# Kernel optimization log

Measured on AMD Instinct MI355X. Metric: run time of the kernel, lower is better.

## Reference

```python
import jax, jax.numpy as jnp
import numpy as np

B, T, D, R = 8, 4096, 512, 1024  # batch, tokens, dim, merges per sequence


def setup_inputs() -> dict:
    key = jax.random.key(0)
    k1, k2 = jax.random.split(key, 2)
    x = jax.random.normal(k1, (B, T, D), jnp.float32)
    W = jax.random.normal(k2, (D, D), jnp.float32) * (1.0 / np.sqrt(D))
    b = jnp.zeros((D,), jnp.float32)
    return {"x": x, "W": W, "b": b}


def _l2norm(v):
    # matches torch F.normalize(p=2, eps=1e-12)
    return v / jnp.maximum(jnp.linalg.norm(v, axis=-1, keepdims=True), 1e-12)


def _scatter_rows(arr, idx, vals):
    # arr: (B, T, d); idx: (B, r); vals: (B, r, d) -> set rows along axis 1
    Bn, _, d = arr.shape
    return arr.at[jnp.arange(Bn)[:, None, None], idx[:, :, None], jnp.arange(d)[None, None, :]].set(vals)


def _tome_forward(x, W, b, r):
    Bn, Tn, d = x.shape
    dst = x[:, 0::2, :]   # even positions
    src = x[:, 1::2, :]   # odd positions
    # cosine similarity bipartite scores: (B, T/2, T/2)
    scores = jnp.einsum('bsd,btd->bst', _l2norm(src), _l2norm(dst))
    best_scores = scores.max(axis=-1)          # (B, T_src)
    best_local = scores.argmax(axis=-1)        # (B, T_src)
    _, top_src = jax.lax.top_k(best_scores, r) # (B, r) src tokens with strongest match
    src_idx = top_src * 2 + 1                  # odd original positions
    dst_idx = jnp.take_along_axis(best_local, top_src, axis=1) * 2  # even original positions
    bidx = jnp.arange(Bn)[:, None]
    merged_away = jnp.zeros((Bn, Tn), bool).at[bidx, src_idx].set(True)

    # --- merge: average src into matched dst, drop src rows ---
    src_vals = jnp.take_along_axis(x, src_idx[:, :, None], axis=1)
    dst_vals = jnp.take_along_axis(x, dst_idx[:, :, None], axis=1)
    x_out = _scatter_rows(x, dst_idx, (src_vals + dst_vals) * 0.5)
    # kept positions in ascending order (stable sort: False before True)
    col = jnp.argsort(merged_away, axis=1, stable=True)[:, :Tn - r]  # (B, T-r)
    merged = jnp.take_along_axis(x_out, col[:, :, None], axis=1)     # (B, T-r, d)

    # --- wrapped dense layer ---
    hidden = merged @ W + b

    # --- unmerge: scatter kept rows back, copy dst value into src slots ---
    out = _scatter_rows(jnp.zeros((Bn, Tn, d), x.dtype), col, hidden)
    dvals = jnp.take_along_axis(out, dst_idx[:, :, None], axis=1)
    out = _scatter_rows(out, src_idx, dvals)
    return out


def reference(x, W, b):
    return _tome_forward(x, W, b, R)
```

## Files before the change

### kernel.cpp

```cpp
#include <hip/hip_runtime.h>
#include <stdint.h>

#define NB   8
#define TOK  4096
#define DIM  512
#define HALF 2048
#define RR   1024

typedef unsigned long long u64;
typedef unsigned int u32;
typedef _Float16 f16;
typedef f16 f16x4 __attribute__((ext_vector_type(4)));
typedef f16 f16x8 __attribute__((ext_vector_type(8)));
typedef float f32x4 __attribute__((ext_vector_type(4)));

#define AS1 __attribute__((address_space(1)))
#define AS3 __attribute__((address_space(3)))
#define GLL16(GP, LP) __builtin_amdgcn_global_load_lds((const AS1 u32*)(GP), (AS3 u32*)(LP), 16, 0, 0)

__device__ __forceinline__ u32 mono_f32(float f) {
    u32 u = __float_as_uint(f);
    return (u & 0x80000000u) ? ~u : (u | 0x80000000u);
}
__device__ __forceinline__ u64 umax64(u64 a, u64 b) { return a > b ? a : b; }

__global__ void k_init(u64* __restrict__ best, u64* __restrict__ wkey) {
    int i = blockIdx.x * 256 + threadIdx.x;
    if (i < NB * HALF) { best[i] = 0ull; wkey[i] = ~0ull; }
}

__global__ void k_prep(const float* __restrict__ x, f16* __restrict__ xh, f16* __restrict__ xl,
                       float* __restrict__ invn) {
    int row  = blockIdx.x * 4 + (threadIdx.x >> 6);
    int lane = threadIdx.x & 63;
    const float* p = x + (size_t)row * DIM + 4 * lane;
    float4 v0 = *(const float4*)p;
    float4 v1 = *(const float4*)(p + 256);
    float va[8] = {v0.x, v0.y, v0.z, v0.w, v1.x, v1.y, v1.z, v1.w};
    f16x4 h0, h1, l0, l1;
#pragma unroll
    for (int e = 0; e < 4; ++e) {
        f16 hh = (f16)va[e];     h0[e] = hh; l0[e] = (f16)(va[e] - (float)hh);
        f16 hh1 = (f16)va[e+4];  h1[e] = hh1; l1[e] = (f16)(va[e+4] - (float)hh1);
    }
    size_t off = (size_t)row * DIM + 4 * lane;
    *(f16x4*)(xh + off)       = h0;
    *(f16x4*)(xh + off + 256) = h1;
    *(f16x4*)(xl + off)       = l0;
    *(f16x4*)(xl + off + 256) = l1;
    float ss = va[0]*va[0] + va[1]*va[1] + va[2]*va[2] + va[3]*va[3]
             + va[4]*va[4] + va[5]*va[5] + va[6]*va[6] + va[7]*va[7];
#pragma unroll
    for (int m = 32; m; m >>= 1) ss += __shfl_xor(ss, m, 64);
    if (lane == 0) invn[row] = 1.0f / fmaxf(sqrtf(ss), 1e-12f);
}

__global__ void k_wsplit(const float* __restrict__ W, f16* __restrict__ Wh, f16* __restrict__ Wl) {
    __shared__ float tile[64][65];
    int k0 = (blockIdx.x >> 3) * 64, n0 = (blockIdx.x & 7) * 64;
    int t = threadIdx.x;
#pragma unroll
    for (int i = 0; i < 16; ++i) {
        int idx = t + 256 * i;
        int r = idx >> 6, c = idx & 63;
        tile[r][c] = W[(size_t)(k0 + r) * DIM + n0 + c];
    }
    __syncthreads();
#pragma unroll
    for (int i = 0; i < 16; ++i) {
        int idx = t + 256 * i;
        int n = idx >> 6, k = idx & 63;
        float v = tile[k][n];
        f16 h = (f16)v;
        Wh[(size_t)(n0 + n) * DIM + k0 + k] = h;
        Wl[(size_t)(n0 + n) * DIM + k0 + k] = (f16)(v - (float)h);
    }
}

__launch_bounds__(256)
__global__ void k_scores(const f16* __restrict__ xh, const f16* __restrict__ xl,
                         const float* __restrict__ invn, u64* __restrict__ best) {
    __shared__ f16 As[128][64];
    __shared__ f16 Bs[128][64];
    int bx = blockIdx.x;
    int b = bx >> 8, sb = (bx >> 4) & 15, tb = bx & 15;
    int tid = threadIdx.x, lane = tid & 63, w = tid >> 6, wr = w >> 1, wc = w & 1;
    int cc = lane >> 4, rm = lane & 15, rm7 = rm & 7;
    f16* Asl = &As[0][0];
    f16* Bsl = &Bs[0][0];

    f32x4 acc[4][4];
#pragma unroll
    for (int i = 0; i < 4; ++i)
#pragma unroll
        for (int j = 0; j < 4; ++j) acc[i][j] = (f32x4){0.f, 0.f, 0.f, 0.f};

    size_t rowA[4], rowB[4];
#pragma unroll
    for (int r = 0; r < 4; ++r) {
        int g = tid + 256 * r;
        int m = g >> 3;
        int chunk = (g & 7) ^ (m & 7);
        rowA[r] = ((size_t)b * TOK + 2 * (sb * 128 + m) + 1) * DIM + 8 * chunk;
        rowB[r] = ((size_t)b * TOK + 2 * (tb * 128 + m)    ) * DIM + 8 * chunk;
    }

    for (int ks = 0; ks < 24; ++ks) {
        int third = ks >> 3, col0 = (ks & 7) << 6;
        const f16* Aa = (third == 1) ? xl : xh;
        const f16* Ba = (third == 2) ? xl : xh;
#pragma unroll
        for (int r = 0; r < 4; ++r) {
            GLL16(Aa + rowA[r] + col0, Asl + (size_t)(256 * r + 64 * w) * 8);
            GLL16(Ba + rowB[r] + col0, Bsl + (size_t)(256 * r + 64 * w) * 8);
        }
        __syncthreads();
        const f16* Abase = Asl + (wr * 64 + rm) * 64;
        const f16* Bbase = Bsl + (wc * 64 + rm) * 64;
#pragma unroll
        for (int kk = 0; kk < 2; ++kk) {
            f16x8 af[4], bf[4];
            int ex = 8 * ((kk * 4 + cc) ^ rm7);
#pragma unroll
            for (int f = 0; f < 4; ++f) {
                af[f] = *(const f16x8*)(Abase + f * 1024 + ex);
                bf[f] = *(const f16x8*)(Bbase + f * 1024 + ex);
            }
#pragma unroll
            for (int i = 0; i < 4; ++i)
#pragma unroll
                for (int j = 0; j < 4; ++j)
                    acc[i][j] = __builtin_amdgcn_mfma_f32_16x16x32_f16(af[i], bf[j], acc[i][j], 0, 0, 0);
        }
        __syncthreads();
    }

    float invd[4];
#pragma unroll
    for (int j = 0; j < 4; ++j) {
        int t = tb * 128 + wc * 64 + j * 16 + rm;
        invd[j] = invn[(size_t)b * TOK + 2 * t];
    }
#pragma unroll
    for (int i = 0; i < 4; ++i) {
#pragma unroll
        for (int r = 0; r < 4; ++r) {
            int s = sb * 128 + wr * 64 + i * 16 + cc * 4 + r;
            float invs = invn[(size_t)b * TOK + 2 * s + 1];
            u64 key = 0;
#pragma unroll
            for (int j = 0; j < 4; ++j) {
                int t = tb * 128 + wc * 64 + j * 16 + rm;
                float sc = acc[i][j][r] * invs * invd[j];
                u64 k = ((u64)mono_f32(sc) << 32) | (u32)(2047 - t);
                key = umax64(key, k);
            }
#pragma unroll
            for (int m = 1; m < 16; m <<= 1) {
                u32 lo = (u32)key, hi = (u32)(key >> 32);
                lo = __shfl_xor(lo, m, 64);
                hi = __shfl_xor(hi, m, 64);
                key = umax64(key, ((u64)hi << 32) | lo);
            }
            if (rm == 0) atomicMax(&best[b * HALF + s], key);
        }
    }
}

__global__ void k_topk(const u64* __restrict__ best, u64* __restrict__ wkey,
                       u32* __restrict__ member, u32* __restrict__ dstmap) {
    __shared__ u32 smono[HALF];
    int b = blockIdx.x >> 4, sc = blockIdx.x & 15;
    int tid = threadIdx.x;
#pragma unroll
    for (int r = 0; r < 8; ++r) { int s = r * 256 + tid; smono[s] = (u32)(best[b * HALF + s] >> 32); }
    __syncthreads();
    int s = sc * 128 + (tid >> 1);
    u32 ms = smono[s];
    int t0 = (tid & 1) * 1024;
    int cnt = 0;
    for (int t = t0; t < t0 + 1024; ++t) {
        u32 mt = smono[t];
        cnt += ((mt > ms) || (mt == ms && t < s)) ? 1 : 0;
    }
    int oth = __shfl_xor(cnt, 1, 64);
    if ((tid & 1) == 0) {
        int rank = cnt + oth;
        u64 k = best[b * HALF + s];
        u32 d = 2047u - (u32)(k & 0xffffffffu);
        dstmap[b * HALF + s] = d;
        u32 mem = (rank < RR) ? 1u : 0u;
        member[b * HALF + s] = mem;
        if (mem) {
            u64 key = (k & 0xffffffff00000000ull) | (u32)(2047 - s);
            atomicMin(&wkey[b * HALF + d], key);
        }
    }
}

__global__ void k_merge2(const float* __restrict__ x, const u64* __restrict__ wkey,
                         f16* __restrict__ xh, f16* __restrict__ xl) {
    int idx = blockIdx.x;
    int b = idx >> 11, d = idx & (HALF - 1);
    u64 wk = wkey[b * HALF + d];
    if (wk == ~0ull) return;
    int s = 2047 - (int)(wk & 0xffffffffu);
    const float* xd = x + ((size_t)b * TOK + 2 * d) * DIM;
    const float* xs = x + ((size_t)b * TOK + 2 * s + 1) * DIM;
    int l0 = threadIdx.x * 8;
    f16x8 h, l;
#pragma unroll
    for (int e = 0; e < 8; ++e) {
        float v = (xd[l0 + e] + xs[l0 + e]) * 0.5f;
        f16 hh = (f16)v;
        h[e] = hh;
        l[e] = (f16)(v - (float)hh);
    }
    size_t off = ((size_t)b * TOK + 2 * d) * DIM + l0;
    *(f16x8*)(xh + off) = h;
    *(f16x8*)(xl + off) = l;
}

__launch_bounds__(256)
__global__ void k_out(const f16* __restrict__ xh, const f16* __restrict__ xl,
                      const f16* __restrict__ Wh, const f16* __restrict__ Wl,
                      const float* __restrict__ bias, float* __restrict__ out) {
    __shared__ f16 As[128][64];
    __shared__ f16 Bs[128][64];
    int bx = blockIdx.x;
    int im = bx >> 2, in = bx & 3;
    int tid = threadIdx.x, lane = tid & 63, w = tid >> 6, wr = w >> 1, wc = w & 1;
    int cc = lane >> 4, rm = lane & 15, rm7 = rm & 7;
    f16* Asl = &As[0][0];
    f16* Bsl = &Bs[0][0];

    f32x4 acc[4][4];
#pragma unroll
    for (int i = 0; i < 4; ++i)
#pragma unroll
        for (int j = 0; j < 4; ++j) acc[i][j] = (f32x4){0.f, 0.f, 0.f, 0.f};

    size_t rowA[4], rowB[4];
#pragma unroll
    for (int r = 0; r < 4; ++r) {
        int g = tid + 256 * r;
        int m = g >> 3;
        int chunk = (g & 7) ^ (m & 7);
        rowA[r] = (size_t)(im * 128 + m) * DIM + 8 * chunk;
        rowB[r] = (size_t)(in * 128 + m) * DIM + 8 * chunk;
    }

    for (int ks = 0; ks < 24; ++ks) {
        int third = ks >> 3, col0 = (ks & 7) << 6;
        const f16* Aa = (third == 1) ? xl : xh;
        const f16* Ba = (third == 2) ? Wl : Wh;
#pragma unroll
        for (int r = 0; r < 4; ++r) {
            GLL16(Aa + rowA[r] + col0, Asl + (size_t)(256 * r + 64 * w) * 8);
            GLL16(Ba + rowB[r] + col0, Bsl + (size_t)(256 * r + 64 * w) * 8);
        }
        __syncthreads();
        const f16* Abase = Asl + (wr * 64 + rm) * 64;
        const f16* Bbase = Bsl + (wc * 64 + rm) * 64;
#pragma unroll
        for (int kk = 0; kk < 2; ++kk) {
            f16x8 af[4], bf[4];
            int ex = 8 * ((kk * 4 + cc) ^ rm7);
#pragma unroll
            for (int f = 0; f < 4; ++f) {
                af[f] = *(const f16x8*)(Abase + f * 1024 + ex);
                bf[f] = *(const f16x8*)(Bbase + f * 1024 + ex);
            }
#pragma unroll
            for (int i = 0; i < 4; ++i)
#pragma unroll
                for (int j = 0; j < 4; ++j)
                    acc[i][j] = __builtin_amdgcn_mfma_f32_16x16x32_f16(af[i], bf[j], acc[i][j], 0, 0, 0);
        }
        __syncthreads();
    }

    float bj[4];
#pragma unroll
    for (int j = 0; j < 4; ++j) bj[j] = bias[in * 128 + wc * 64 + j * 16 + rm];
#pragma unroll
    for (int i = 0; i < 4; ++i) {
#pragma unroll
        for (int r = 0; r < 4; ++r) {
            int gm = im * 128 + wr * 64 + i * 16 + cc * 4 + r;
#pragma unroll
            for (int j = 0; j < 4; ++j) {
                int n = in * 128 + wc * 64 + j * 16 + rm;
                out[(size_t)gm * DIM + n] = acc[i][j][r] + bj[j];
            }
        }
    }
}

__global__ void k_fix(const u32* __restrict__ member, const u32* __restrict__ dstmap,
                      float* __restrict__ out) {
    int idx = blockIdx.x;
    if (!member[idx]) return;
    int b = idx >> 11, s = idx & (HALF - 1);
    const float* sp = out + ((size_t)b * TOK + 2 * (size_t)dstmap[idx]) * DIM;
    float*       dp = out + ((size_t)b * TOK + 2 * (size_t)s + 1) * DIM;
    int l = threadIdx.x;
    *(float4*)(dp + 4 * l) = *(const float4*)(sp + 4 * l);
}

extern "C" void kernel_launch(void* const* d_in, const int* in_sizes, int n_in,
                              void* d_out, int out_size, void* d_ws, size_t ws_size,
                              hipStream_t stream) {
    const float* x    = (const float*)d_in[0];
    const float* W    = (const float*)d_in[1];
    const float* bias = (const float*)d_in[2];
    float* out = (float*)d_out;

    char* ws = (char*)d_ws;
    f16*   xh     = (f16*)(ws);
    f16*   xl     = (f16*)(ws + (32u << 20));
    f16*   Wh     = (f16*)(ws + (64u << 20));
    f16*   Wl     = (f16*)(ws + (64u << 20) + (512u << 10));
    float* invn   = (float*)(ws + (65u << 20));
    u64*   best   = (u64*)(ws + (65u << 20) + (128u << 10));
    u64*   wkey   = (u64*)(ws + (65u << 20) + (256u << 10));
    u32*   dstmap = (u32*)(ws + (65u << 20) + (384u << 10));
    u32*   member = (u32*)(ws + (65u << 20) + (448u << 10));

    hipLaunchKernelGGL(k_init,   dim3(64),    dim3(256), 0, stream, best, wkey);
    hipLaunchKernelGGL(k_prep,   dim3(8192),  dim3(256), 0, stream, x, xh, xl, invn);
    hipLaunchKernelGGL(k_wsplit, dim3(64),    dim3(256), 0, stream, W, Wh, Wl);
    hipLaunchKernelGGL(k_scores, dim3(2048),  dim3(256), 0, stream, xh, xl, invn, best);
    hipLaunchKernelGGL(k_topk,   dim3(128),   dim3(256), 0, stream, best, wkey, member, dstmap);
    hipLaunchKernelGGL(k_merge2, dim3(16384), dim3(64),  0, stream, x, wkey, xh, xl);
    hipLaunchKernelGGL(k_out,    dim3(1024),  dim3(256), 0, stream, xh, xl, Wh, Wl, bias, out);
    hipLaunchKernelGGL(k_fix,    dim3(16384), dim3(128), 0, stream, member, dstmap, out);
}
```

Baseline: 390.4 us.

## Double-buffer GEMM K-loops, fuse prep kernels, and fold unmerge copy into output GEMM

Merges the init, x-split and W-split kernels into one launch. Both GEMMs now stage the hi and lo halves of each K-slice together into double-buffered LDS, so the next slice loads while the current one computes, and one sync per step replaces the separate three-pass loop. The output GEMM also redirects each merged-away source row to read its dst row directly, which removes the k_fix pass. The cost is four times the LDS per block, which may reduce occupancy, and some duplicated GEMM rows for the redirected sources.

```diff
diff --git a/kernel.cpp b/kernel.cpp
--- a/kernel.cpp
+++ b/kernel.cpp
@@ -24,70 +24,100 @@
 }
 __device__ __forceinline__ u64 umax64(u64 a, u64 b) { return a > b ? a : b; }
 
-__global__ void k_init(u64* __restrict__ best, u64* __restrict__ wkey) {
-    int i = blockIdx.x * 256 + threadIdx.x;
-    if (i < NB * HALF) { best[i] = 0ull; wkey[i] = ~0ull; }
-}
-
-__global__ void k_prep(const float* __restrict__ x, f16* __restrict__ xh, f16* __restrict__ xl,
-                       float* __restrict__ invn) {
-    int row  = blockIdx.x * 4 + (threadIdx.x >> 6);
-    int lane = threadIdx.x & 63;
-    const float* p = x + (size_t)row * DIM + 4 * lane;
-    float4 v0 = *(const float4*)p;
-    float4 v1 = *(const float4*)(p + 256);
-    float va[8] = {v0.x, v0.y, v0.z, v0.w, v1.x, v1.y, v1.z, v1.w};
-    f16x4 h0, h1, l0, l1;
-#pragma unroll
-    for (int e = 0; e < 4; ++e) {
-        f16 hh = (f16)va[e];     h0[e] = hh; l0[e] = (f16)(va[e] - (float)hh);
-        f16 hh1 = (f16)va[e+4];  h1[e] = hh1; l1[e] = (f16)(va[e+4] - (float)hh1);
-    }
-    size_t off = (size_t)row * DIM + 4 * lane;
-    *(f16x4*)(xh + off)       = h0;
-    *(f16x4*)(xh + off + 256) = h1;
-    *(f16x4*)(xl + off)       = l0;
-    *(f16x4*)(xl + off + 256) = l1;
-    float ss = va[0]*va[0] + va[1]*va[1] + va[2]*va[2] + va[3]*va[3]
-             + va[4]*va[4] + va[5]*va[5] + va[6]*va[6] + va[7]*va[7];
-#pragma unroll
-    for (int m = 32; m; m >>= 1) ss += __shfl_xor(ss, m, 64);
-    if (lane == 0) invn[row] = 1.0f / fmaxf(sqrtf(ss), 1e-12f);
-}
-
-__global__ void k_wsplit(const float* __restrict__ W, f16* __restrict__ Wh, f16* __restrict__ Wl) {
+__global__ void k_pre(const float* __restrict__ x, f16* __restrict__ xh, f16* __restrict__ xl,
+                      float* __restrict__ invn, const float* __restrict__ W,
+                      f16* __restrict__ Wh, f16* __restrict__ Wl,
+                      u64* __restrict__ best, u64* __restrict__ wkey) {
     __shared__ float tile[64][65];
-    int k0 = (blockIdx.x >> 3) * 64, n0 = (blockIdx.x & 7) * 64;
-    int t = threadIdx.x;
-#pragma unroll
-    for (int i = 0; i < 16; ++i) {
-        int idx = t + 256 * i;
-        int r = idx >> 6, c = idx & 63;
-        tile[r][c] = W[(size_t)(k0 + r) * DIM + n0 + c];
-    }
-    __syncthreads();
-#pragma unroll
-    for (int i = 0; i < 16; ++i) {
-        int idx = t + 256 * i;
-        int n = idx >> 6, k = idx & 63;
-        float v = tile[k][n];
-        f16 h = (f16)v;
-        Wh[(size_t)(n0 + n) * DIM + k0 + k] = h;
-        Wl[(size_t)(n0 + n) * DIM + k0 + k] = (f16)(v - (float)h);
-    }
-}
+    int bid = blockIdx.x, tid = threadIdx.x;
+    if (bid < 8192) {
+        int row  = bid * 4 + (tid >> 6);
+        int lane = tid & 63;
+        const float* p = x + (size_t)row * DIM + 4 * lane;
+        float4 v0 = *(const float4*)p;
+        float4 v1 = *(const float4*)(p + 256);
+        float va[8] = {v0.x, v0.y, v0.z, v0.w, v1.x, v1.y, v1.z, v1.w};
+        f16x4 h0, h1, l0, l1;
+#pragma unroll
+        for (int e = 0; e < 4; ++e) {
+            f16 hh = (f16)va[e];     h0[e] = hh;  l0[e] = (f16)(va[e] - (float)hh);
+            f16 hh1 = (f16)va[e+4];  h1[e] = hh1; l1[e] = (f16)(va[e+4] - (float)hh1);
+        }
+        size_t off = (size_t)row * DIM + 4 * lane;
+        *(f16x4*)(xh + off)       = h0;
+        *(f16x4*)(xh + off + 256) = h1;
+        *(f16x4*)(xl + off)       = l0;
+        *(f16x4*)(xl + off + 256) = l1;
+        float ss = va[0]*va[0] + va[1]*va[1] + va[2]*va[2] + va[3]*va[3]
+                 + va[4]*va[4] + va[5]*va[5] + va[6]*va[6] + va[7]*va[7];
+#pragma unroll
+        for (int m = 32; m; m >>= 1) ss += __shfl_xor(ss, m, 64);
+        if (lane == 0) invn[row] = 1.0f / fmaxf(sqrtf(ss), 1e-12f);
+    } else if (bid < 8256) {
+        int wb = bid - 8192;
+        int k0 = (wb >> 3) * 64, n0 = (wb & 7) * 64;
+#pragma unroll
+        for (int i = 0; i < 16; ++i) {
+            int idx = tid + 256 * i;
+            int r = idx >> 6, c = idx & 63;
+            tile[r][c] = W[(size_t)(k0 + r) * DIM + n0 + c];
+        }
+        __syncthreads();
+#pragma unroll
+        for (int i = 0; i < 16; ++i) {
+            int idx = tid + 256 * i;
+            int n = idx >> 6, k = idx & 63;
+            float v = tile[k][n];
+            f16 h = (f16)v;
+            Wh[(size_t)(n0 + n) * DIM + k0 + k] = h;
+            Wl[(size_t)(n0 + n) * DIM + k0 + k] = (f16)(v - (float)h);
+        }
+    } else {
+        int i = (bid - 8256) * 256 + tid;
+        if (i < NB * HALF) { best[i] = 0ull; wkey[i] = ~0ull; }
+    }
+}
+
+
+#define STAGE4(AP, BP, LB, COL) { \
+  _Pragma("unroll") for (int r_ = 0; r_ < 4; ++r_) { \
+    size_t d_ = (size_t)(256 * r_ + 64 * w) * 8; \
+    GLL16((AP##h) + rowA[r_] + (COL), (LB) + d_); \
+    GLL16((AP##l) + rowA[r_] + (COL), (LB) + 8192 + d_); \
+    GLL16((BP##h) + rowB[r_] + (COL), (LB) + 16384 + d_); \
+    GLL16((BP##l) + rowB[r_] + (COL), (LB) + 24576 + d_); \
+  } }
+
+#define COMPUTE_STEP(LB) { \
+  const f16* Ah_ = (LB) + (wr * 64 + rm) * 64; \
+  const f16* Bh_ = (LB) + 16384 + (wc * 64 + rm) * 64; \
+  _Pragma("unroll") for (int kk = 0; kk < 2; ++kk) { \
+    int ex = 8 * ((kk * 4 + cc) ^ rm7); \
+    f16x8 ah[4], al[4], bh[4], bl[4]; \
+    _Pragma("unroll") for (int f = 0; f < 4; ++f) { \
+      ah[f] = *(const f16x8*)(Ah_ + f * 1024 + ex); \
+      al[f] = *(const f16x8*)(Ah_ + 8192 + f * 1024 + ex); \
+      bh[f] = *(const f16x8*)(Bh_ + f * 1024 + ex); \
+      bl[f] = *(const f16x8*)(Bh_ + 8192 + f * 1024 + ex); \
+    } \
+    _Pragma("unroll") for (int i = 0; i < 4; ++i) \
+      _Pragma("unroll") for (int j = 0; j < 4; ++j) { \
+        acc[i][j] = __builtin_amdgcn_mfma_f32_16x16x32_f16(ah[i], bh[j], acc[i][j], 0, 0, 0); \
+        acc[i][j] = __builtin_amdgcn_mfma_f32_16x16x32_f16(al[i], bh[j], acc[i][j], 0, 0, 0); \
+        acc[i][j] = __builtin_amdgcn_mfma_f32_16x16x32_f16(ah[i], bl[j], acc[i][j], 0, 0, 0); \
+      } \
+  } }
 
 __launch_bounds__(256)
 __global__ void k_scores(const f16* __restrict__ xh, const f16* __restrict__ xl,
                          const float* __restrict__ invn, u64* __restrict__ best) {
-    __shared__ f16 As[128][64];
-    __shared__ f16 Bs[128][64];
+    __shared__ __align__(16) f16 L[2][4][128][64];
     int bx = blockIdx.x;
     int b = bx >> 8, sb = (bx >> 4) & 15, tb = bx & 15;
     int tid = threadIdx.x, lane = tid & 63, w = tid >> 6, wr = w >> 1, wc = w & 1;
     int cc = lane >> 4, rm = lane & 15, rm7 = rm & 7;
-    f16* Asl = &As[0][0];
-    f16* Bsl = &Bs[0][0];
+    f16* L0 = &L[0][0][0][0];
+    f16* L1 = &L[1][0][0][0];
 
     f32x4 acc[4][4];
 #pragma unroll
@@ -105,33 +135,14 @@
         rowB[r] = ((size_t)b * TOK + 2 * (tb * 128 + m)    ) * DIM + 8 * chunk;
     }
 
-    for (int ks = 0; ks < 24; ++ks) {
-        int third = ks >> 3, col0 = (ks & 7) << 6;
-        const f16* Aa = (third == 1) ? xl : xh;
-        const f16* Ba = (third == 2) ? xl : xh;
-#pragma unroll
-        for (int r = 0; r < 4; ++r) {
-            GLL16(Aa + rowA[r] + col0, Asl + (size_t)(256 * r + 64 * w) * 8);
-            GLL16(Ba + rowB[r] + col0, Bsl + (size_t)(256 * r + 64 * w) * 8);
-        }
-        __syncthreads();
-        const f16* Abase = Asl + (wr * 64 + rm) * 64;
-        const f16* Bbase = Bsl + (wc * 64 + rm) * 64;
-#pragma unroll
-        for (int kk = 0; kk < 2; ++kk) {
-            f16x8 af[4], bf[4];
-            int ex = 8 * ((kk * 4 + cc) ^ rm7);
-#pragma unroll
-            for (int f = 0; f < 4; ++f) {
-                af[f] = *(const f16x8*)(Abase + f * 1024 + ex);
-                bf[f] = *(const f16x8*)(Bbase + f * 1024 + ex);
-            }
-#pragma unroll
-            for (int i = 0; i < 4; ++i)
-#pragma unroll
-                for (int j = 0; j < 4; ++j)
-                    acc[i][j] = __builtin_amdgcn_mfma_f32_16x16x32_f16(af[i], bf[j], acc[i][j], 0, 0, 0);
-        }
+    STAGE4(x, x, L0, 0)
+    __syncthreads();
+#pragma unroll 1
+    for (int ks = 0; ks < 8; ++ks) {
+        f16* Lc = (ks & 1) ? L1 : L0;
+        f16* Ln = (ks & 1) ? L0 : L1;
+        if (ks < 7) { int coln = (ks + 1) << 6; STAGE4(x, x, Ln, coln) }
+        COMPUTE_STEP(Lc)
         __syncthreads();
     }
 
@@ -224,15 +235,15 @@
 __launch_bounds__(256)
 __global__ void k_out(const f16* __restrict__ xh, const f16* __restrict__ xl,
                       const f16* __restrict__ Wh, const f16* __restrict__ Wl,
-                      const float* __restrict__ bias, float* __restrict__ out) {
-    __shared__ f16 As[128][64];
-    __shared__ f16 Bs[128][64];
+                      const float* __restrict__ bias, const u32* __restrict__ member,
+                      const u32* __restrict__ dstmap, float* __restrict__ out) {
+    __shared__ __align__(16) f16 L[2][4][128][64];
     int bx = blockIdx.x;
     int im = bx >> 2, in = bx & 3;
     int tid = threadIdx.x, lane = tid & 63, w = tid >> 6, wr = w >> 1, wc = w & 1;
     int cc = lane >> 4, rm = lane & 15, rm7 = rm & 7;
-    f16* Asl = &As[0][0];
-    f16* Bsl = &Bs[0][0];
+    f16* L0 = &L[0][0][0][0];
+    f16* L1 = &L[1][0][0][0];
 
     f32x4 acc[4][4];
 #pragma unroll
@@ -246,37 +257,24 @@
         int g = tid + 256 * r;
         int m = g >> 3;
         int chunk = (g & 7) ^ (m & 7);
-        rowA[r] = (size_t)(im * 128 + m) * DIM + 8 * chunk;
+        int grow = im * 128 + m;
+        int b_ = grow >> 12, tok = grow & (TOK - 1);
+        if (tok & 1) {
+            int s = tok >> 1;
+            if (member[b_ * HALF + s]) tok = 2 * (int)dstmap[b_ * HALF + s];
+        }
+        rowA[r] = (((size_t)b_ << 12) + tok) * DIM + 8 * chunk;
         rowB[r] = (size_t)(in * 128 + m) * DIM + 8 * chunk;
     }
 
-    for (int ks = 0; ks < 24; ++ks) {
-        int third = ks >> 3, col0 = (ks & 7) << 6;
-        const f16* Aa = (third == 1) ? xl : xh;
-        const f16* Ba = (third == 2) ? Wl : Wh;
-#pragma unroll
-        for (int r = 0; r < 4; ++r) {
-            GLL16(Aa + rowA[r] + col0, Asl + (size_t)(256 * r + 64 * w) * 8);
-            GLL16(Ba + rowB[r] + col0, Bsl + (size_t)(256 * r + 64 * w) * 8);
-        }
-        __syncthreads();
-        const f16* Abase = Asl + (wr * 64 + rm) * 64;
-        const f16* Bbase = Bsl + (wc * 64 + rm) * 64;
-#pragma unroll
-        for (int kk = 0; kk < 2; ++kk) {
-            f16x8 af[4], bf[4];
-            int ex = 8 * ((kk * 4 + cc) ^ rm7);
-#pragma unroll
-            for (int f = 0; f < 4; ++f) {
-                af[f] = *(const f16x8*)(Abase + f * 1024 + ex);
-                bf[f] = *(const f16x8*)(Bbase + f * 1024 + ex);
-            }
-#pragma unroll
-            for (int i = 0; i < 4; ++i)
-#pragma unroll
-                for (int j = 0; j < 4; ++j)
-                    acc[i][j] = __builtin_amdgcn_mfma_f32_16x16x32_f16(af[i], bf[j], acc[i][j], 0, 0, 0);
-        }
+    STAGE4(x, W, L0, 0)
+    __syncthreads();
+#pragma unroll 1
+    for (int ks = 0; ks < 8; ++ks) {
+        f16* Lc = (ks & 1) ? L1 : L0;
+        f16* Ln = (ks & 1) ? L0 : L1;
+        if (ks < 7) { int coln = (ks + 1) << 6; STAGE4(x, W, Ln, coln) }
+        COMPUTE_STEP(Lc)
         __syncthreads();
     }
 
@@ -295,17 +293,6 @@
             }
         }
     }
-}
-
-__global__ void k_fix(const u32* __restrict__ member, const u32* __restrict__ dstmap,
-                      float* __restrict__ out) {
-    int idx = blockIdx.x;
-    if (!member[idx]) return;
-    int b = idx >> 11, s = idx & (HALF - 1);
-    const float* sp = out + ((size_t)b * TOK + 2 * (size_t)dstmap[idx]) * DIM;
-    float*       dp = out + ((size_t)b * TOK + 2 * (size_t)s + 1) * DIM;
-    int l = threadIdx.x;
-    *(float4*)(dp + 4 * l) = *(const float4*)(sp + 4 * l);
 }
 
 extern "C" void kernel_launch(void* const* d_in, const int* in_sizes, int n_in,
@@ -327,12 +314,9 @@
     u32*   dstmap = (u32*)(ws + (65u << 20) + (384u << 10));
     u32*   member = (u32*)(ws + (65u << 20) + (448u << 10));
 
-    hipLaunchKernelGGL(k_init,   dim3(64),    dim3(256), 0, stream, best, wkey);
-    hipLaunchKernelGGL(k_prep,   dim3(8192),  dim3(256), 0, stream, x, xh, xl, invn);
-    hipLaunchKernelGGL(k_wsplit, dim3(64),    dim3(256), 0, stream, W, Wh, Wl);
+    hipLaunchKernelGGL(k_pre,    dim3(8320),  dim3(256), 0, stream, x, xh, xl, invn, W, Wh, Wl, best, wkey);
     hipLaunchKernelGGL(k_scores, dim3(2048),  dim3(256), 0, stream, xh, xl, invn, best);
     hipLaunchKernelGGL(k_topk,   dim3(128),   dim3(256), 0, stream, best, wkey, member, dstmap);
     hipLaunchKernelGGL(k_merge2, dim3(16384), dim3(64),  0, stream, x, wkey, xh, xl);
-    hipLaunchKernelGGL(k_out,    dim3(1024),  dim3(256), 0, stream, xh, xl, Wh, Wl, bias, out);
-    hipLaunchKernelGGL(k_fix,    dim3(16384), dim3(128), 0, stream, member, dstmap, out);
-}
+    hipLaunchKernelGGL(k_out,    dim3(1024),  dim3(256), 0, stream, xh, xl, Wh, Wl, bias, member, dstmap, out);
+}
```

After: 390.0 us. Within noise of the previous version (-0.1%).
